# Performance work log

Measured on AMD Instinct MI355X. Metric: run time of the kernel, lower is better.

## Reference

```python
import jax, jax.numpy as jnp
import numpy as np

# Plane axes from generate_planes(); projection uses their inverses (permutation matrices).
_PLANES = np.array([[[1, 0, 0], [0, 1, 0], [0, 0, 1]],
                    [[1, 0, 0], [0, 0, 1], [0, 1, 0]],
                    [[0, 0, 1], [1, 0, 0], [0, 1, 0]]], dtype=np.float32)
_INV_PLANES = np.linalg.inv(_PLANES)  # [3,3,3]


def _grid_sample_2d(feat, grid):
    """Bilinear grid_sample, padding_mode='zeros', align_corners=False.
    feat: [C,H,W], grid: [M,2] with (x,y) in normalized coords. Returns [C,M]."""
    C, H, W = feat.shape
    x = ((grid[:, 0] + 1.0) * W - 1.0) * 0.5  # [M] pixel coords
    y = ((grid[:, 1] + 1.0) * H - 1.0) * 0.5
    x0 = jnp.floor(x)
    y0 = jnp.floor(y)
    wx = x - x0  # weight of right/bottom neighbor
    wy = y - y0
    x0i = x0.astype(jnp.int32)
    y0i = y0.astype(jnp.int32)
    x1i = x0i + 1
    y1i = y0i + 1

    def corner(xi, yi):
        valid = (xi >= 0) & (xi < W) & (yi >= 0) & (yi < H)
        xc = jnp.clip(xi, 0, W - 1)
        yc = jnp.clip(yi, 0, H - 1)
        v = feat[:, yc, xc]  # [C, M] gather
        return v * valid.astype(feat.dtype)

    v00 = corner(x0i, y0i)
    v10 = corner(x1i, y0i)
    v01 = corner(x0i, y1i)
    v11 = corner(x1i, y1i)
    out = (v00 * (1.0 - wx) * (1.0 - wy)
           + v10 * wx * (1.0 - wy)
           + v01 * (1.0 - wx) * wy
           + v11 * wx * wy)
    return out  # [C, M]


def setup_inputs() -> dict:
    key = jax.random.key(0)
    k1, k2, k3 = jax.random.split(key, 3)
    N, P, C, H, W, M = 4, 3, 32, 256, 256, 500000
    planes = jax.random.normal(k1, (N, P, C, H, W), dtype=jnp.float32)
    sample_coordinates = jax.random.uniform(k2, (N, M, 3), dtype=jnp.float32,
                                            minval=-1.0, maxval=1.0)
    sample_directions = jax.random.normal(k3, (N, M, 3), dtype=jnp.float32)
    return {"planes": planes, "sample_coordinates": sample_coordinates,
            "sample_directions": sample_directions}


def reference(planes, sample_coordinates, sample_directions):
    # ImportanceRenderer.run_model: project -> grid_sample per plane -> mean over planes.
    N, n_planes, C, H, W = planes.shape
    M = sample_coordinates.shape[1]
    inv = jnp.asarray(_INV_PLANES, dtype=sample_coordinates.dtype)  # [P,3,3]
    # torch.bmm(coords, inv_planes): [N,P,M,3] @ [P,3,3] -> take first 2 dims
    proj = jnp.einsum('nmi,pij->npmj', sample_coordinates, inv)[..., :2]  # [N,P,M,2]
    feats = planes.reshape(N * n_planes, C, H, W)
    grids = proj.reshape(N * n_planes, M, 2)
    sampled = jax.vmap(_grid_sample_2d)(feats, grids)  # [N*P, C, M]
    sampled = sampled.reshape(N, n_planes, C, M).transpose(0, 1, 3, 2)  # [N,P,M,C]
    return sampled.mean(axis=1)  # [N, M, C]
```

## Files before the change

kernel.cpp:

```cpp
#include <hip/hip_runtime.h>
#include <hip/hip_fp16.h>


constexpr int Cc = 32, Hh = 256, Ww = 256, Pp = 3, Nn = 4;
constexpr int HWPIX = Hh * Ww;
constexpr int NCO   = 4096;
constexpr int CAP   = 256;
constexpr int TAILB = 64;

typedef float f32x4 __attribute__((ext_vector_type(4)));

__device__ inline unsigned spread3(unsigned x) {
    x &= 0x3FFu;
    x = (x | (x << 16)) & 0x030000FFu;
    x = (x | (x << 8))  & 0x0300F00Fu;
    x = (x | (x << 4))  & 0x030C30C3u;
    x = (x | (x << 2))  & 0x09249249u;
    return x;
}
__device__ inline unsigned coarse_key(float cx, float cy, float cz) {
    const int a = min(max((int)((cx + 1.0f) * 8.0f), 0), 15);
    const int b = min(max((int)((cy + 1.0f) * 8.0f), 0), 15);
    const int c = min(max((int)((cz + 1.0f) * 8.0f), 0), 15);
    return spread3((unsigned)a) | (spread3((unsigned)b) << 1) | (spread3((unsigned)c) << 2);
}

__global__ __launch_bounds__(256) void zero_u32(unsigned* __restrict__ p, int n)
{
    const int i = blockIdx.x * 256 + threadIdx.x;
    if (i < n) p[i] = 0u;
}

__global__ __launch_bounds__(256) void transpose_chw_hwc_h(
    const float* __restrict__ in, __half* __restrict__ out)
{
    __shared__ float lds[Cc * 257];
    const int slice = blockIdx.y;
    const int pix0  = blockIdx.x * 256;
    const int t     = threadIdx.x;

    const float* src = in + (size_t)slice * Cc * HWPIX + pix0 + t;
    #pragma unroll
    for (int c = 0; c < Cc; ++c)
        lds[c * 257 + t] = src[(size_t)c * HWPIX];
    __syncthreads();

    uint4* dst = reinterpret_cast<uint4*>(
        out + (size_t)slice * HWPIX * Cc + (size_t)pix0 * Cc);
    #pragma unroll
    for (int k = 0; k < 4; ++k) {
        const int idx = k * 256 + t;
        const int pix = idx >> 2;
        const int c0  = (idx & 3) * 8;
        unsigned r[4];
        #pragma unroll
        for (int j = 0; j < 4; ++j) {
            const __half h0 = __float2half(lds[(c0 + 2 * j + 0) * 257 + pix]);
            const __half h1 = __float2half(lds[(c0 + 2 * j + 1) * 257 + pix]);
            r[j] = (unsigned)__half_as_ushort(h0)
                 | ((unsigned)__half_as_ushort(h1) << 16);
        }
        dst[idx] = make_uint4(r[0], r[1], r[2], r[3]);
    }
}

__global__ __launch_bounds__(256) void bin_scatter(
    const float* __restrict__ coords, unsigned* __restrict__ count,
    unsigned* __restrict__ tailcnt, unsigned* __restrict__ bin,
    unsigned* __restrict__ tail, int M)
{
    const int m = blockIdx.x * 256 + threadIdx.x;
    const int n = blockIdx.y;
    if (m >= M) return;
    const float* cp = coords + ((size_t)n * M + m) * 3;
    const unsigned k = coarse_key(cp[0], cp[1], cp[2]);
    const unsigned r = atomicAdd(&count[n * NCO + k], 1u);
    if (r < CAP) {
        __builtin_nontemporal_store((unsigned)m,
            bin + (((size_t)n * NCO + k) << 8) + r);
    } else {
        const unsigned tt = atomicAdd(&tailcnt[n], 1u);
        tail[(size_t)n * M + tt] = (unsigned)m;
    }
}

__device__ __forceinline__ void gather_one(
    const __half* __restrict__ tp, const float* __restrict__ coords,
    float* __restrict__ out, int n, int m, int quad, int M)
{
    const float* cp = coords + ((size_t)n * M + m) * 3;
    const float cx = cp[0], cy = cp[1], cz = cp[2];

    const uint4* addr[12];
    __half2 wh[12];

    #pragma unroll
    for (int p = 0; p < 3; ++p) {
        const float gxc = (p == 2) ? cz : cx;
        const float gyc = (p == 0) ? cy : ((p == 1) ? cz : cx);
        const float x = ((gxc + 1.0f) * 256.0f - 1.0f) * 0.5f;
        const float y = ((gyc + 1.0f) * 256.0f - 1.0f) * 0.5f;
        const float x0f = floorf(x), y0f = floorf(y);
        const float wx = x - x0f, wy = y - y0f;
        const int x0 = (int)x0f, y0 = (int)y0f;
        const int x1 = x0 + 1,   y1 = y0 + 1;
        const bool vx0 = (unsigned)x0 < 256u;
        const bool vx1 = (unsigned)x1 < 256u;
        const bool vy0 = (unsigned)y0 < 256u;
        const bool vy1 = (unsigned)y1 < 256u;
        const int cx0 = min(max(x0, 0), 255), cx1 = min(max(x1, 0), 255);
        const int cy0 = min(max(y0, 0), 255), cy1 = min(max(y1, 0), 255);

        const float w00 = ((vx0 && vy0) ? 1.f : 0.f) * (1.f - wx) * (1.f - wy);
        const float w10 = ((vx1 && vy0) ? 1.f : 0.f) * wx * (1.f - wy);
        const float w01 = ((vx0 && vy1) ? 1.f : 0.f) * (1.f - wx) * wy;
        const float w11 = ((vx1 && vy1) ? 1.f : 0.f) * wx * wy;
        wh[p * 4 + 0] = __float2half2_rn(w00);
        wh[p * 4 + 1] = __float2half2_rn(w10);
        wh[p * 4 + 2] = __float2half2_rn(w01);
        wh[p * 4 + 3] = __float2half2_rn(w11);

        const uint4* base = reinterpret_cast<const uint4*>(
            tp + (size_t)(n * 3 + p) * HWPIX * Cc);
        addr[p * 4 + 0] = base + (size_t)((cy0 << 8) + cx0) * 4 + quad;
        addr[p * 4 + 1] = base + (size_t)((cy0 << 8) + cx1) * 4 + quad;
        addr[p * 4 + 2] = base + (size_t)((cy1 << 8) + cx0) * 4 + quad;
        addr[p * 4 + 3] = base + (size_t)((cy1 << 8) + cx1) * 4 + quad;
    }

    uint4 rv[12];
    #pragma unroll
    for (int j = 0; j < 12; ++j) rv[j] = *addr[j];

    float accx[8];
    #pragma unroll
    for (int i = 0; i < 8; ++i) accx[i] = 0.f;

    #pragma unroll
    for (int p = 0; p < 3; ++p) {
        __half2 a0 = __float2half2_rn(0.f), a1 = a0, a2 = a0, a3 = a0;
        #pragma unroll
        for (int c = 0; c < 4; ++c) {
            const uint4 v = rv[p * 4 + c];
            const __half2 w = wh[p * 4 + c];
            a0 = __hfma2(*reinterpret_cast<const __half2*>(&v.x), w, a0);
            a1 = __hfma2(*reinterpret_cast<const __half2*>(&v.y), w, a1);
            a2 = __hfma2(*reinterpret_cast<const __half2*>(&v.z), w, a2);
            a3 = __hfma2(*reinterpret_cast<const __half2*>(&v.w), w, a3);
        }
        const float2 f0 = __half22float2(a0);
        const float2 f1 = __half22float2(a1);
        const float2 f2 = __half22float2(a2);
        const float2 f3 = __half22float2(a3);
        accx[0] += f0.x; accx[1] += f0.y;
        accx[2] += f1.x; accx[3] += f1.y;
        accx[4] += f2.x; accx[5] += f2.y;
        accx[6] += f3.x; accx[7] += f3.y;
    }

    constexpr float third = 1.0f / 3.0f;
    f32x4 o0, o1;
    o0.x = accx[0] * third; o0.y = accx[1] * third;
    o0.z = accx[2] * third; o0.w = accx[3] * third;
    o1.x = accx[4] * third; o1.y = accx[5] * third;
    o1.z = accx[6] * third; o1.w = accx[7] * third;

    f32x4* op = reinterpret_cast<f32x4*>(out + ((size_t)n * M + m) * Cc);
    __builtin_nontemporal_store(o0, op + quad * 2 + 0);
    __builtin_nontemporal_store(o1, op + quad * 2 + 1);
}

__global__ __launch_bounds__(256) void gather_cells(
    const __half* __restrict__ tp, const unsigned* __restrict__ count,
    const unsigned* __restrict__ tailcnt, const unsigned* __restrict__ bin,
    const unsigned* __restrict__ tail, const float* __restrict__ coords,
    float* __restrict__ out, int M, int nwg)
{
    int bid = blockIdx.x;
    {
        const int q = nwg >> 3, r = nwg & 7;
        const int xcd = bid & 7, i = bid >> 3;
        bid = (xcd < r ? xcd * (q + 1) : r * (q + 1) + (xcd - r) * q) + i;
    }
    constexpr int PER_N = NCO + TAILB;
    const int n  = bid / PER_N;
    const int cb = bid - n * PER_N;
    const int t  = threadIdx.x;
    const int ls = t >> 2;
    const int quad = t & 3;

    if (cb < NCO) {
        unsigned c = count[n * NCO + cb];
        c = (c > (unsigned)CAP) ? (unsigned)CAP : c;
        const unsigned* bp = bin + (((size_t)n * NCO + cb) << 8);
        for (unsigned base = 0; base < c; base += 64) {
            const unsigned j = base + ls;
            if (j < c)
                gather_one(tp, coords, out, n, (int)bp[j], quad, M);
        }
    } else {
        unsigned tc = tailcnt[n];
        if (tc > (unsigned)M) tc = (unsigned)M;
        for (unsigned s = (unsigned)(cb - NCO) * 64 + ls; s < tc;
             s += (unsigned)TAILB * 64)
            gather_one(tp, coords, out, n, (int)tail[(size_t)n * M + s], quad, M);
    }
}

__global__ __launch_bounds__(256) void triplane_gather_hwc8h(
    const __half* __restrict__ tp, const float* __restrict__ coords,
    float* __restrict__ out, int M)
{
    const int gid   = blockIdx.x * 256 + threadIdx.x;
    const int m     = gid >> 3;
    const int chunk = gid & 7;
    const int n     = blockIdx.y;
    if (m >= M) return;

    const float* cp = coords + ((size_t)n * M + m) * 3;
    const float cx = cp[0], cy = cp[1], cz = cp[2];

    const uint2* addr[12];
    float w[12];

    #pragma unroll
    for (int p = 0; p < 3; ++p) {
        const float gxc = (p == 2) ? cz : cx;
        const float gyc = (p == 0) ? cy : ((p == 1) ? cz : cx);
        const float x = ((gxc + 1.0f) * 256.0f - 1.0f) * 0.5f;
        const float y = ((gyc + 1.0f) * 256.0f - 1.0f) * 0.5f;
        const float x0f = floorf(x), y0f = floorf(y);
        const float wx = x - x0f, wy = y - y0f;
        const int x0 = (int)x0f, y0 = (int)y0f;
        const int x1 = x0 + 1,   y1 = y0 + 1;
        const bool vx0 = (unsigned)x0 < 256u;
        const bool vx1 = (unsigned)x1 < 256u;
        const bool vy0 = (unsigned)y0 < 256u;
        const bool vy1 = (unsigned)y1 < 256u;
        const int cx0 = min(max(x0, 0), 255), cx1 = min(max(x1, 0), 255);
        const int cy0 = min(max(y0, 0), 255), cy1 = min(max(y1, 0), 255);

        w[p * 4 + 0] = ((vx0 && vy0) ? 1.f : 0.f) * (1.f - wx) * (1.f - wy);
        w[p * 4 + 1] = ((vx1 && vy0) ? 1.f : 0.f) * wx * (1.f - wy);
        w[p * 4 + 2] = ((vx0 && vy1) ? 1.f : 0.f) * (1.f - wx) * wy;
        w[p * 4 + 3] = ((vx1 && vy1) ? 1.f : 0.f) * wx * wy;

        const uint2* base = reinterpret_cast<const uint2*>(
            tp + (size_t)(n * 3 + p) * HWPIX * Cc);
        addr[p * 4 + 0] = base + (size_t)((cy0 << 8) + cx0) * 8 + chunk;
        addr[p * 4 + 1] = base + (size_t)((cy0 << 8) + cx1) * 8 + chunk;
        addr[p * 4 + 2] = base + (size_t)((cy1 << 8) + cx0) * 8 + chunk;
        addr[p * 4 + 3] = base + (size_t)((cy1 << 8) + cx1) * 8 + chunk;
    }

    uint2 rv[12];
    #pragma unroll
    for (int j = 0; j < 12; ++j) rv[j] = *addr[j];

    float4 acc = make_float4(0.f, 0.f, 0.f, 0.f);
    #pragma unroll
    for (int j = 0; j < 12; ++j) {
        const __half2 h0 = *reinterpret_cast<const __half2*>(&rv[j].x);
        const __half2 h1 = *reinterpret_cast<const __half2*>(&rv[j].y);
        const float2 f0 = __half22float2(h0);
        const float2 f1 = __half22float2(h1);
        acc.x += w[j] * f0.x;
        acc.y += w[j] * f0.y;
        acc.z += w[j] * f1.x;
        acc.w += w[j] * f1.y;
    }

    constexpr float third = 1.0f / 3.0f;
    acc.x *= third; acc.y *= third; acc.z *= third; acc.w *= third;

    float4* op = reinterpret_cast<float4*>(out + ((size_t)n * M + m) * Cc);
    op[chunk] = acc;
}

__global__ __launch_bounds__(256) void triplane_gather_chw(
    const float* __restrict__ planes, const float* __restrict__ coords,
    float* __restrict__ out, int M)
{
    const int m = blockIdx.x * 256 + threadIdx.x;
    const int n = blockIdx.y;
    if (m >= M) return;

    const float* cp = coords + ((size_t)n * M + m) * 3;
    const float cx = cp[0], cy = cp[1], cz = cp[2];

    int   off[3][4];
    float w[3][4];
    #pragma unroll
    for (int p = 0; p < 3; ++p) {
        const float gxc = (p == 2) ? cz : cx;
        const float gyc = (p == 0) ? cy : ((p == 1) ? cz : cx);
        const float x = ((gxc + 1.0f) * 256.0f - 1.0f) * 0.5f;
        const float y = ((gyc + 1.0f) * 256.0f - 1.0f) * 0.5f;
        const float x0f = floorf(x), y0f = floorf(y);
        const float wx = x - x0f, wy = y - y0f;
        const int x0 = (int)x0f, y0 = (int)y0f;
        const int x1 = x0 + 1,   y1 = y0 + 1;
        const bool vx0 = (unsigned)x0 < 256u, vx1 = (unsigned)x1 < 256u;
        const bool vy0 = (unsigned)y0 < 256u, vy1 = (unsigned)y1 < 256u;
        const int cx0 = min(max(x0, 0), 255), cx1 = min(max(x1, 0), 255);
        const int cy0 = min(max(y0, 0), 255), cy1 = min(max(y1, 0), 255);
        off[p][0] = (cy0 << 8) + cx0;  w[p][0] = ((vx0 && vy0) ? 1.f : 0.f) * (1.f - wx) * (1.f - wy);
        off[p][1] = (cy0 << 8) + cx1;  w[p][1] = ((vx1 && vy0) ? 1.f : 0.f) * wx * (1.f - wy);
        off[p][2] = (cy1 << 8) + cx0;  w[p][2] = ((vx0 && vy1) ? 1.f : 0.f) * (1.f - wx) * wy;
        off[p][3] = (cy1 << 8) + cx1;  w[p][3] = ((vx1 && vy1) ? 1.f : 0.f) * wx * wy;
    }

    float* op = out + ((size_t)n * M + m) * Cc;
    constexpr float third = 1.0f / 3.0f;
    for (int c = 0; c < Cc; ++c) {
        float a = 0.f;
        #pragma unroll
        for (int p = 0; p < 3; ++p) {
            const float* b = planes + ((size_t)(n * 3 + p) * Cc + c) * HWPIX;
            a += w[p][0] * b[off[p][0]] + w[p][1] * b[off[p][1]]
               + w[p][2] * b[off[p][2]] + w[p][3] * b[off[p][3]];
        }
        op[c] = a * third;
    }
}

extern "C" void kernel_launch(void* const* d_in, const int* in_sizes, int n_in,
                              void* d_out, int out_size, void* d_ws, size_t ws_size,
                              hipStream_t stream)
{
    const float* planes = (const float*)d_in[0];
    const float* coords = (const float*)d_in[1];
    float* out = (float*)d_out;

    const int M = in_sizes[1] / (Nn * 3);

    auto align256 = [](size_t x) { return (x + 255) & ~(size_t)255; };
    const size_t tph_bytes  = align256((size_t)Nn * Pp * HWPIX * Cc * sizeof(__half));
    const size_t bin_bytes  = align256((size_t)Nn * NCO * CAP * sizeof(unsigned));
    const size_t tail_bytes = align256((size_t)Nn * M * sizeof(unsigned));
    const size_t cnt_bytes  = align256((size_t)Nn * NCO * sizeof(unsigned));
    const size_t tc_bytes   = align256((size_t)Nn * sizeof(unsigned));

    if (ws_size >= tph_bytes + bin_bytes + tail_bytes + cnt_bytes + tc_bytes) {
        char* p = (char*)d_ws;
        __half*   tp      = (__half*)p;   p += tph_bytes;
        unsigned* bin     = (unsigned*)p; p += bin_bytes;
        unsigned* tail    = (unsigned*)p; p += tail_bytes;
        unsigned* count   = (unsigned*)p; p += cnt_bytes;
        unsigned* tailcnt = (unsigned*)p;

        const int nz = Nn * NCO + Nn;
        zero_u32<<<(nz + 255) / 256, 256, 0, stream>>>(count, nz);

        transpose_chw_hwc_h<<<dim3(HWPIX / 256, Nn * Pp), 256, 0, stream>>>(planes, tp);
        bin_scatter<<<dim3((M + 255) / 256, Nn), 256, 0, stream>>>(
            coords, count, tailcnt, bin, tail, M);

        const int nwg = Nn * (NCO + TAILB);
        gather_cells<<<nwg, 256, 0, stream>>>(tp, count, tailcnt, bin, tail,
                                              coords, out, M, nwg);
    } else if (ws_size >= tph_bytes) {
        __half* tp = (__half*)d_ws;
        transpose_chw_hwc_h<<<dim3(HWPIX / 256, Nn * Pp), 256, 0, stream>>>(planes, tp);
        const int gx = (M * 8 + 255) / 256;
        triplane_gather_hwc8h<<<dim3(gx, Nn), 256, 0, stream>>>(tp, coords, out, M);
    } else {
        const int gx = (M + 255) / 256;
        triplane_gather_chw<<<dim3(gx, Nn), 256, 0, stream>>>(planes, coords, out, M);
    }
}
```

Baseline: 321.8 us.

## Split each sample across eight lanes, one x-corner per lane pair

Each sample point now uses eight threads instead of four. Each half of the group fetches only one x-side of the bilinear corners, six 16-byte loads instead of twelve. The two halves' partial sums are combined with a lane shuffle, and each thread stores one float4 of output. This raises memory-level parallelism and cuts per-thread registers, at the cost of twice the thread count, duplicated coordinate and weight math, and an extra shuffle step. The bin store also changes from a nontemporal store to a plain store.

```diff
diff --git a/kernel.cpp b/kernel.cpp
--- a/kernel.cpp
+++ b/kernel.cpp
@@ -76,23 +76,22 @@
     const unsigned k = coarse_key(cp[0], cp[1], cp[2]);
     const unsigned r = atomicAdd(&count[n * NCO + k], 1u);
     if (r < CAP) {
-        __builtin_nontemporal_store((unsigned)m,
-            bin + (((size_t)n * NCO + k) << 8) + r);
+        bin[(((size_t)n * NCO + k) << 8) + r] = (unsigned)m;
     } else {
         const unsigned tt = atomicAdd(&tailcnt[n], 1u);
         tail[(size_t)n * M + tt] = (unsigned)m;
     }
 }
 
-__device__ __forceinline__ void gather_one(
+__device__ __forceinline__ void gather_one8(
     const __half* __restrict__ tp, const float* __restrict__ coords,
-    float* __restrict__ out, int n, int m, int quad, int M)
+    float* __restrict__ out, int n, int m, int quad, int side, int M)
 {
     const float* cp = coords + ((size_t)n * M + m) * 3;
     const float cx = cp[0], cy = cp[1], cz = cp[2];
 
-    const uint4* addr[12];
-    __half2 wh[12];
+    const uint4* addr[6];
+    __half2 wh[6];
 
     #pragma unroll
     for (int p = 0; p < 3; ++p) {
@@ -111,26 +110,22 @@
         const int cx0 = min(max(x0, 0), 255), cx1 = min(max(x1, 0), 255);
         const int cy0 = min(max(y0, 0), 255), cy1 = min(max(y1, 0), 255);
 
-        const float w00 = ((vx0 && vy0) ? 1.f : 0.f) * (1.f - wx) * (1.f - wy);
-        const float w10 = ((vx1 && vy0) ? 1.f : 0.f) * wx * (1.f - wy);
-        const float w01 = ((vx0 && vy1) ? 1.f : 0.f) * (1.f - wx) * wy;
-        const float w11 = ((vx1 && vy1) ? 1.f : 0.f) * wx * wy;
-        wh[p * 4 + 0] = __float2half2_rn(w00);
-        wh[p * 4 + 1] = __float2half2_rn(w10);
-        wh[p * 4 + 2] = __float2half2_rn(w01);
-        wh[p * 4 + 3] = __float2half2_rn(w11);
-
+        const float wxs = side ? (vx1 ? wx : 0.f) : (vx0 ? (1.f - wx) : 0.f);
+        const float wy0 = vy0 ? (1.f - wy) : 0.f;
+        const float wy1 = vy1 ? wy : 0.f;
+        wh[p * 2 + 0] = __float2half2_rn(wxs * wy0);
+        wh[p * 2 + 1] = __float2half2_rn(wxs * wy1);
+
+        const int xs = side ? cx1 : cx0;
         const uint4* base = reinterpret_cast<const uint4*>(
             tp + (size_t)(n * 3 + p) * HWPIX * Cc);
-        addr[p * 4 + 0] = base + (size_t)((cy0 << 8) + cx0) * 4 + quad;
-        addr[p * 4 + 1] = base + (size_t)((cy0 << 8) + cx1) * 4 + quad;
-        addr[p * 4 + 2] = base + (size_t)((cy1 << 8) + cx0) * 4 + quad;
-        addr[p * 4 + 3] = base + (size_t)((cy1 << 8) + cx1) * 4 + quad;
-    }
-
-    uint4 rv[12];
-    #pragma unroll
-    for (int j = 0; j < 12; ++j) rv[j] = *addr[j];
+        addr[p * 2 + 0] = base + (size_t)((cy0 << 8) + xs) * 4 + quad;
+        addr[p * 2 + 1] = base + (size_t)((cy1 << 8) + xs) * 4 + quad;
+    }
+
+    uint4 rv[6];
+    #pragma unroll
+    for (int j = 0; j < 6; ++j) rv[j] = *addr[j];
 
     float accx[8];
     #pragma unroll
@@ -140,9 +135,9 @@
     for (int p = 0; p < 3; ++p) {
         __half2 a0 = __float2half2_rn(0.f), a1 = a0, a2 = a0, a3 = a0;
         #pragma unroll
-        for (int c = 0; c < 4; ++c) {
-            const uint4 v = rv[p * 4 + c];
-            const __half2 w = wh[p * 4 + c];
+        for (int yc = 0; yc < 2; ++yc) {
+            const uint4 v = rv[p * 2 + yc];
+            const __half2 w = wh[p * 2 + yc];
             a0 = __hfma2(*reinterpret_cast<const __half2*>(&v.x), w, a0);
             a1 = __hfma2(*reinterpret_cast<const __half2*>(&v.y), w, a1);
             a2 = __hfma2(*reinterpret_cast<const __half2*>(&v.z), w, a2);
@@ -158,16 +153,17 @@
         accx[6] += f3.x; accx[7] += f3.y;
     }
 
+    #pragma unroll
+    for (int i = 0; i < 8; ++i) accx[i] += __shfl_xor(accx[i], 4);
+
     constexpr float third = 1.0f / 3.0f;
-    f32x4 o0, o1;
-    o0.x = accx[0] * third; o0.y = accx[1] * third;
-    o0.z = accx[2] * third; o0.w = accx[3] * third;
-    o1.x = accx[4] * third; o1.y = accx[5] * third;
-    o1.z = accx[6] * third; o1.w = accx[7] * third;
+    const int h = side * 4;
+    f32x4 o;
+    o.x = accx[h + 0] * third; o.y = accx[h + 1] * third;
+    o.z = accx[h + 2] * third; o.w = accx[h + 3] * third;
 
     f32x4* op = reinterpret_cast<f32x4*>(out + ((size_t)n * M + m) * Cc);
-    __builtin_nontemporal_store(o0, op + quad * 2 + 0);
-    __builtin_nontemporal_store(o1, op + quad * 2 + 1);
+    __builtin_nontemporal_store(o, op + quad * 2 + side);
 }
 
 __global__ __launch_bounds__(256) void gather_cells(
@@ -186,24 +182,26 @@
     const int n  = bid / PER_N;
     const int cb = bid - n * PER_N;
     const int t  = threadIdx.x;
-    const int ls = t >> 2;
+    const int ls   = t >> 3;
     const int quad = t & 3;
+    const int side = (t >> 2) & 1;
 
     if (cb < NCO) {
         unsigned c = count[n * NCO + cb];
         c = (c > (unsigned)CAP) ? (unsigned)CAP : c;
         const unsigned* bp = bin + (((size_t)n * NCO + cb) << 8);
-        for (unsigned base = 0; base < c; base += 64) {
+        for (unsigned base = 0; base < c; base += 32) {
             const unsigned j = base + ls;
             if (j < c)
-                gather_one(tp, coords, out, n, (int)bp[j], quad, M);
+                gather_one8(tp, coords, out, n, (int)bp[j], quad, side, M);
         }
     } else {
         unsigned tc = tailcnt[n];
         if (tc > (unsigned)M) tc = (unsigned)M;
-        for (unsigned s = (unsigned)(cb - NCO) * 64 + ls; s < tc;
-             s += (unsigned)TAILB * 64)
-            gather_one(tp, coords, out, n, (int)tail[(size_t)n * M + s], quad, M);
+        for (unsigned s = (unsigned)(cb - NCO) * 32 + ls; s < tc;
+             s += (unsigned)TAILB * 32)
+            gather_one8(tp, coords, out, n, (int)tail[(size_t)n * M + s],
+                        quad, side, M);
     }
 }
 
```

After: 301.5 us. -6.3%, faster.
